# Kernel optimization log

Hardware: AMD Instinct MI355X
Metric: run time of the kernel (lower is better)

## Reference

```python
import jax, jax.numpy as jnp
import numpy as np

N_NODES = 50000
N_EDGES = 800000
F_IN, D1, N_CLS = 128, 128, 64


def gcn_conv(x, W, b, src, dst, n):
    # x: [N, Fin] -> linear transform then normalized scatter-add aggregation
    h = x @ W  # [N, Fout]
    deg = jnp.zeros((n,), h.dtype).at[dst].add(jnp.ones((dst.shape[0],), h.dtype))
    dis = jnp.where(deg > 0, jax.lax.rsqrt(jnp.maximum(deg, 1.0)), 0.0)  # deg^-1/2, inf->0
    norm = dis[src] * dis[dst]  # [E_tot]
    msgs = norm[:, None] * h[src]  # gather source features, scale by sym norm
    out = jax.ops.segment_sum(msgs, dst, num_segments=n)  # scatter-add to targets
    return out + b


def setup_inputs() -> dict:
    key = jax.random.key(0)
    ks = jax.random.split(key, 6)
    x = jax.random.normal(ks[0], (N_NODES, F_IN), dtype=jnp.float32)
    edge_index = jax.random.randint(ks[1], (2, N_EDGES), 0, N_NODES, dtype=jnp.int64)
    W1 = jax.random.normal(ks[2], (F_IN, D1), dtype=jnp.float32) / np.sqrt(F_IN)
    b1 = jnp.zeros((D1,), dtype=jnp.float32)
    W2 = jax.random.normal(ks[3], (D1, N_CLS), dtype=jnp.float32) / np.sqrt(D1)
    b2 = jnp.zeros((N_CLS,), dtype=jnp.float32)
    return {"x": x, "edge_index": edge_index, "W1": W1, "b1": b1, "W2": W2, "b2": b2}


def reference(x, edge_index, W1, b1, W2, b2):
    n = x.shape[0]
    loops = jnp.arange(n, dtype=edge_index.dtype)
    src = jnp.concatenate([edge_index[0], loops])  # add self-loops (PyG default)
    dst = jnp.concatenate([edge_index[1], loops])
    h = gcn_conv(x, W1, b1, src, dst, n)
    h = jax.nn.relu(h)
    # F.dropout(training=self.training) is identity in eval mode
    out = gcn_conv(h, W2, b2, src, dst, n)
    return out
```

## Files before the change

### kernel.cpp

```cpp
#include <hip/hip_runtime.h>

#define NN 50000
#define NE 800000
#define CAP 64
#define NPAD 50176
#define SLICE 6250

typedef unsigned int   u32;
typedef unsigned short u16;
typedef __attribute__((ext_vector_type(8))) short short8;
typedef __attribute__((ext_vector_type(4))) float f32x4;

__device__ inline u16 f2bf(float f) {
    u32 u = __float_as_uint(f);
    return (u16)((u + 0x7FFF + ((u >> 16) & 1)) >> 16);
}
__device__ inline float bfval(u16 h) { return __uint_as_float(((u32)h) << 16); }
__device__ inline float bf_lo(u32 u) { return __uint_as_float(u << 16); }
__device__ inline float bf_hi(u32 u) { return __uint_as_float(u & 0xFFFF0000u); }


__global__ __launch_bounds__(256) void build_ell(const int* __restrict__ ei,
                                                 int* __restrict__ cnt,
                                                 u16* __restrict__ ell) {
    const int s  = blockIdx.x & 7;
    const int g  = blockIdx.x >> 3;
    const int ng = gridDim.x >> 3;
    const int lo = s * SLICE, hi = lo + SLICE;
    for (int e0 = (g * 256 + (int)threadIdx.x) * 4; e0 < NE; e0 += ng * 1024) {
        int4 d4 = *(const int4*)(ei + NE + e0);
        int dv[4] = {d4.x, d4.y, d4.z, d4.w};
#pragma unroll
        for (int k = 0; k < 4; ++k) {
            int d = dv[k];
            if (d >= lo && d < hi) {
                int src = ei[e0 + k];
                int sh = k & 1;
                int pos = atomicAdd(&cnt[sh * NPAD + d], 1);
                if (pos < 32) ell[d * CAP + sh * 32 + pos] = (u16)src;
            }
        }
    }
}


__global__ __launch_bounds__(256) void prep_w(const float* __restrict__ W1,
                                              const float* __restrict__ W2,
                                              u16* __restrict__ W1h, u16* __restrict__ W1l,
                                              u16* __restrict__ W2h, u16* __restrict__ W2l,
                                              int* __restrict__ cnt) {
    int i = blockIdx.x * 256 + threadIdx.x;
    for (int z = i; z < 2 * NPAD; z += 32768) cnt[z] = 0;
    const float* W; u16 *Dh, *Dl; int NOUT, idx;
    if (i < 16384) { W = W1; Dh = W1h; Dl = W1l; NOUT = 128; idx = i; }
    else           { idx = i - 16384; if (idx >= 8192) return;
                     W = W2; Dh = W2h; Dl = W2l; NOUT = 64; }
    int j = idx & 7, l = (idx >> 3) & 63, kc = (idx >> 9) & 3, t = idx >> 11;
    int k = kc * 32 + (l >> 4) * 8 + j;
    int n = t * 16 + (l & 15);
    float w = W[k * NOUT + n];
    u16 h = f2bf(w);
    Dh[idx] = h;
    Dl[idx] = f2bf(w - bfval(h));
}


template <int NOUT>
__global__ __launch_bounds__(256) void gemm_mfma(const float* __restrict__ A,
                                                 const u16* __restrict__ Wh,
                                                 const u16* __restrict__ Wl,
                                                 u16* __restrict__ C, int M) {
    constexpr int NT = NOUT / 16;
    const int tid = threadIdx.x;
    const int w = tid >> 6, l = tid & 63;
    const int m = l & 15, q = l >> 4;

    int arow = blockIdx.x * 64 + w * 16 + m;
    const float* Ar = A + (size_t)min(arow, M - 1) * 128;

    f32x4 acc[NT] = {};

#pragma unroll
    for (int kc = 0; kc < 4; ++kc) {
        float p[8];
        *(float4*)&p[0] = *(const float4*)(Ar + kc * 32 + q * 8);
        *(float4*)&p[4] = *(const float4*)(Ar + kc * 32 + q * 8 + 4);
        short8 ah, al;
#pragma unroll
        for (int j = 0; j < 8; ++j) {
            u16 h = f2bf(p[j]);
            ah[j] = (short)h;
            al[j] = (short)f2bf(p[j] - bfval(h));
        }
#pragma unroll
        for (int t = 0; t < NT; ++t) {
            size_t bo = ((size_t)(t * 4 + kc) * 64 + l) * 8;
            short8 bh = *(const short8*)(Wh + bo);
            short8 bl = *(const short8*)(Wl + bo);
            acc[t] = __builtin_amdgcn_mfma_f32_16x16x32_bf16(ah, bh, acc[t], 0, 0, 0);
            acc[t] = __builtin_amdgcn_mfma_f32_16x16x32_bf16(al, bh, acc[t], 0, 0, 0);
            acc[t] = __builtin_amdgcn_mfma_f32_16x16x32_bf16(ah, bl, acc[t], 0, 0, 0);
        }
    }

    int growbase = blockIdx.x * 64 + w * 16 + q * 4;
#pragma unroll
    for (int t = 0; t < NT; ++t)
#pragma unroll
        for (int r = 0; r < 4; ++r) {
            int grow = growbase + r;
            if (grow < M) C[(size_t)grow * NOUT + t * 16 + m] = f2bf(acc[t][r]);
        }
}


__global__ __launch_bounds__(256) void gemm_mfma_bf(const u16* __restrict__ A,
                                                    const u16* __restrict__ Wh,
                                                    const u16* __restrict__ Wl,
                                                    u16* __restrict__ C, int M) {
    constexpr int NT = 4;
    const int tid = threadIdx.x;
    const int w = tid >> 6, l = tid & 63;
    const int m = l & 15, q = l >> 4;

    int arow = blockIdx.x * 64 + w * 16 + m;
    const u16* Ar = A + (size_t)min(arow, M - 1) * 128;

    f32x4 acc[NT] = {};

#pragma unroll
    for (int kc = 0; kc < 4; ++kc) {
        short8 ah = *(const short8*)(Ar + kc * 32 + q * 8);
#pragma unroll
        for (int t = 0; t < NT; ++t) {
            size_t bo = ((size_t)(t * 4 + kc) * 64 + l) * 8;
            short8 bh = *(const short8*)(Wh + bo);
            short8 bl = *(const short8*)(Wl + bo);
            acc[t] = __builtin_amdgcn_mfma_f32_16x16x32_bf16(ah, bh, acc[t], 0, 0, 0);
            acc[t] = __builtin_amdgcn_mfma_f32_16x16x32_bf16(ah, bl, acc[t], 0, 0, 0);
        }
    }

    int growbase = blockIdx.x * 64 + w * 16 + q * 4;
#pragma unroll
    for (int t = 0; t < NT; ++t)
#pragma unroll
        for (int r = 0; r < 4; ++r) {
            int grow = growbase + r;
            if (grow < M) C[(size_t)grow * 64 + t * 16 + m] = f2bf(acc[t][r]);
        }
}


template <int F, bool RELU, bool OUTBF>
__global__ __launch_bounds__(256) void aggregate(const u16* __restrict__ H,
                                                 const u16* __restrict__ ell,
                                                 const int* __restrict__ cnt,
                                                 const float* __restrict__ bias,
                                                 void* __restrict__ outp) {
    const int tid = threadIdx.x;
    const int node = (int)((blockIdx.x * 256 + tid) >> 6);
    if (node >= NN) return;
    const int lane = tid & 63;

    const int c0r = cnt[node], c1r = cnt[NPAD + node];
    const int c0 = min(c0r, 32), c1 = min(c1r, 32);
    const int ne = min(c0 + c1, 63);
    const float di = rsqrtf((float)(c0r + c1r + 1));
    int slot = (lane < c0) ? lane : 32 + (lane - c0);
    int   s_l = (lane < ne) ? (int)ell[(size_t)node * CAP + slot] : node;
    float n_l = (lane <= ne)
                    ? rsqrtf((float)(cnt[s_l] + cnt[NPAD + s_l] + 1)) * di
                    : 0.0f;

    constexpr int G = (F == 128) ? 4 : 8;
    constexpr int L = 64 / G;
    const int g = lane / L;
    const int ci = lane & (L - 1);

    const int m = ne + 1;
    const int mPad = (m + 2 * G - 1) & ~(2 * G - 1);

    float acc[8] = {0, 0, 0, 0, 0, 0, 0, 0};
    for (int j = 0; j < mPad; j += 2 * G) {
        int   sA = __shfl(s_l, j + g);
        float nA = __shfl(n_l, j + g);
        int   sB = __shfl(s_l, j + G + g);
        float nB = __shfl(n_l, j + G + g);
        uint4 vA = *(const uint4*)(H + (size_t)sA * F + ci * 8);
        uint4 vB = *(const uint4*)(H + (size_t)sB * F + ci * 8);
        acc[0] += nA * bf_lo(vA.x); acc[1] += nA * bf_hi(vA.x);
        acc[2] += nA * bf_lo(vA.y); acc[3] += nA * bf_hi(vA.y);
        acc[4] += nA * bf_lo(vA.z); acc[5] += nA * bf_hi(vA.z);
        acc[6] += nA * bf_lo(vA.w); acc[7] += nA * bf_hi(vA.w);
        acc[0] += nB * bf_lo(vB.x); acc[1] += nB * bf_hi(vB.x);
        acc[2] += nB * bf_lo(vB.y); acc[3] += nB * bf_hi(vB.y);
        acc[4] += nB * bf_lo(vB.z); acc[5] += nB * bf_hi(vB.z);
        acc[6] += nB * bf_lo(vB.w); acc[7] += nB * bf_hi(vB.w);
    }

#pragma unroll
    for (int i = 0; i < 8; ++i) {
        if (F == 64) acc[i] += __shfl_xor(acc[i], 8);
        acc[i] += __shfl_xor(acc[i], 16);
        acc[i] += __shfl_xor(acc[i], 32);
    }

    const int active = (F == 128) ? 32 : 16;
    if (lane < active) {
        int part, c0i;
        if (F == 128) { part = lane >> 4;       c0i = (lane & 15) * 8 + part * 4; }
        else          { part = (lane >> 3) & 1; c0i = (lane & 7) * 8 + part * 4; }
        float4 b4 = *(const float4*)(bias + c0i);
        float4 o = make_float4(acc[part * 4 + 0] + b4.x, acc[part * 4 + 1] + b4.y,
                               acc[part * 4 + 2] + b4.z, acc[part * 4 + 3] + b4.w);
        if (RELU) { o.x = fmaxf(o.x, 0.f); o.y = fmaxf(o.y, 0.f);
                    o.z = fmaxf(o.z, 0.f); o.w = fmaxf(o.w, 0.f); }
        if (OUTBF) {
            u16* out = (u16*)outp;
            *(ushort4*)(out + (size_t)node * F + c0i) =
                make_ushort4(f2bf(o.x), f2bf(o.y), f2bf(o.z), f2bf(o.w));
        } else {
            float* out = (float*)outp;
            *(float4*)(out + (size_t)node * F + c0i) = o;
        }
    }
}


extern "C" void kernel_launch(void* const* d_in, const int* in_sizes, int n_in,
                              void* d_out, int out_size, void* d_ws, size_t ws_size,
                              hipStream_t stream) {
    const float* x  = (const float*)d_in[0];
    const int*   ei = (const int*)d_in[1];
    const float* W1 = (const float*)d_in[2];
    const float* b1 = (const float*)d_in[3];
    const float* W2 = (const float*)d_in[4];
    const float* b2 = (const float*)d_in[5];
    float* out = (float*)d_out;

    char* ws = (char*)d_ws;
    size_t off = 0;
    int* cnt = (int*)ws;                     off += (size_t)2 * NPAD * 4;
    u16* ell = (u16*)(ws + off);             off += (size_t)NN * CAP * 2;
    off = (off + 255) & ~(size_t)255;
    u16* W1h = (u16*)(ws + off);             off += 16384 * 2;
    u16* W1l = (u16*)(ws + off);             off += 16384 * 2;
    u16* W2h = (u16*)(ws + off);             off += 8192 * 2;
    u16* W2l = (u16*)(ws + off);             off += 8192 * 2;
    off = (off + 255) & ~(size_t)255;
    u16* Hbf = (u16*)(ws + off);             off += (size_t)NN * 128 * 2;
    u16* Abf = (u16*)(ws + off);             off += (size_t)NN * 128 * 2;

    prep_w<<<128, 256, 0, stream>>>(W1, W2, W1h, W1l, W2h, W2l, cnt);
    build_ell<<<1600, 256, 0, stream>>>(ei, cnt, ell);

    gemm_mfma<128><<<(NN + 63) / 64, 256, 0, stream>>>(x, W1h, W1l, Hbf, NN);
    aggregate<128, true, true><<<(NN + 3) / 4, 256, 0, stream>>>(Hbf, ell, cnt, b1, Abf);

    gemm_mfma_bf<<<(NN + 63) / 64, 256, 0, stream>>>(Abf, W2h, W2l, Hbf, NN);
    aggregate<64, false, false><<<(NN + 3) / 4, 256, 0, stream>>>(Hbf, ell, cnt, b2, out);
}
```

Measured before the change: 196.9 us.

## Fuse all GCN stages into one cooperative persistent kernel with grid syncs

Replaces the six separate launches with a single cooperative kernel that uses grid-wide syncs between stages. Half the blocks build the ELL adjacency while the other half run the first GEMM at the same time, and the later stages loop over tiles in persistent-block fashion. The aim is to remove launch gaps and overlap the atomic-heavy graph build with MFMA work. The cost is four grid barriers and a grid capped at 512 blocks, which may reduce occupancy and latency hiding in the gather-heavy aggregation.

Measured after the change: 520.7 us. 164% more time.

```diff
diff --git a/kernel.cpp b/kernel.cpp
--- a/kernel.cpp
+++ b/kernel.cpp
@@ -1,10 +1,14 @@
 #include <hip/hip_runtime.h>
+#include <hip/hip_cooperative_groups.h>
+
+namespace cg = cooperative_groups;
 
 #define NN 50000
 #define NE 800000
 #define CAP 64
 #define NPAD 50176
 #define SLICE 6250
+#define NTILE 782
 
 typedef unsigned int   u32;
 typedef unsigned short u16;
@@ -20,66 +24,44 @@
 __device__ inline float bf_hi(u32 u) { return __uint_as_float(u & 0xFFFF0000u); }
 
 
-__global__ __launch_bounds__(256) void build_ell(const int* __restrict__ ei,
-                                                 int* __restrict__ cnt,
-                                                 u16* __restrict__ ell) {
-    const int s  = blockIdx.x & 7;
-    const int g  = blockIdx.x >> 3;
-    const int ng = gridDim.x >> 3;
+__device__ inline void dev_build(int b, int BB, int tid,
+                                 const int* __restrict__ ei,
+                                 int* __restrict__ cnt,
+                                 u16* __restrict__ ell) {
+    const int s  = b & 7;
+    const int g  = b >> 3;
+    const int ng = BB >> 3;
     const int lo = s * SLICE, hi = lo + SLICE;
-    for (int e0 = (g * 256 + (int)threadIdx.x) * 4; e0 < NE; e0 += ng * 1024) {
+    for (int e0 = (g * 256 + tid) * 4; e0 < NE; e0 += ng * 1024) {
         int4 d4 = *(const int4*)(ei + NE + e0);
+        int4 s4 = *(const int4*)(ei + e0);
         int dv[4] = {d4.x, d4.y, d4.z, d4.w};
+        int sv[4] = {s4.x, s4.y, s4.z, s4.w};
 #pragma unroll
         for (int k = 0; k < 4; ++k) {
             int d = dv[k];
             if (d >= lo && d < hi) {
-                int src = ei[e0 + k];
                 int sh = k & 1;
                 int pos = atomicAdd(&cnt[sh * NPAD + d], 1);
-                if (pos < 32) ell[d * CAP + sh * 32 + pos] = (u16)src;
+                if (pos < 32) ell[d * CAP + sh * 32 + pos] = (u16)sv[k];
             }
         }
     }
 }
 
 
-__global__ __launch_bounds__(256) void prep_w(const float* __restrict__ W1,
-                                              const float* __restrict__ W2,
-                                              u16* __restrict__ W1h, u16* __restrict__ W1l,
-                                              u16* __restrict__ W2h, u16* __restrict__ W2l,
-                                              int* __restrict__ cnt) {
-    int i = blockIdx.x * 256 + threadIdx.x;
-    for (int z = i; z < 2 * NPAD; z += 32768) cnt[z] = 0;
-    const float* W; u16 *Dh, *Dl; int NOUT, idx;
-    if (i < 16384) { W = W1; Dh = W1h; Dl = W1l; NOUT = 128; idx = i; }
-    else           { idx = i - 16384; if (idx >= 8192) return;
-                     W = W2; Dh = W2h; Dl = W2l; NOUT = 64; }
-    int j = idx & 7, l = (idx >> 3) & 63, kc = (idx >> 9) & 3, t = idx >> 11;
-    int k = kc * 32 + (l >> 4) * 8 + j;
-    int n = t * 16 + (l & 15);
-    float w = W[k * NOUT + n];
-    u16 h = f2bf(w);
-    Dh[idx] = h;
-    Dl[idx] = f2bf(w - bfval(h));
-}
-
-
-template <int NOUT>
-__global__ __launch_bounds__(256) void gemm_mfma(const float* __restrict__ A,
-                                                 const u16* __restrict__ Wh,
-                                                 const u16* __restrict__ Wl,
-                                                 u16* __restrict__ C, int M) {
-    constexpr int NT = NOUT / 16;
-    const int tid = threadIdx.x;
+__device__ inline void dev_gemm1_tile(int t, int tid,
+                                      const float* __restrict__ A,
+                                      const u16* __restrict__ Wh,
+                                      const u16* __restrict__ Wl,
+                                      u16* __restrict__ C) {
     const int w = tid >> 6, l = tid & 63;
     const int m = l & 15, q = l >> 4;
 
-    int arow = blockIdx.x * 64 + w * 16 + m;
-    const float* Ar = A + (size_t)min(arow, M - 1) * 128;
-
-    f32x4 acc[NT] = {};
-
+    int arow = t * 64 + w * 16 + m;
+    const float* Ar = A + (size_t)min(arow, NN - 1) * 128;
+
+    f32x4 acc[8] = {};
 #pragma unroll
     for (int kc = 0; kc < 4; ++kc) {
         float p[8];
@@ -93,75 +75,69 @@
             al[j] = (short)f2bf(p[j] - bfval(h));
         }
 #pragma unroll
-        for (int t = 0; t < NT; ++t) {
-            size_t bo = ((size_t)(t * 4 + kc) * 64 + l) * 8;
+        for (int t2 = 0; t2 < 8; ++t2) {
+            size_t bo = ((size_t)(t2 * 4 + kc) * 64 + l) * 8;
             short8 bh = *(const short8*)(Wh + bo);
             short8 bl = *(const short8*)(Wl + bo);
-            acc[t] = __builtin_amdgcn_mfma_f32_16x16x32_bf16(ah, bh, acc[t], 0, 0, 0);
-            acc[t] = __builtin_amdgcn_mfma_f32_16x16x32_bf16(al, bh, acc[t], 0, 0, 0);
-            acc[t] = __builtin_amdgcn_mfma_f32_16x16x32_bf16(ah, bl, acc[t], 0, 0, 0);
-        }
-    }
-
-    int growbase = blockIdx.x * 64 + w * 16 + q * 4;
-#pragma unroll
-    for (int t = 0; t < NT; ++t)
+            acc[t2] = __builtin_amdgcn_mfma_f32_16x16x32_bf16(ah, bh, acc[t2], 0, 0, 0);
+            acc[t2] = __builtin_amdgcn_mfma_f32_16x16x32_bf16(al, bh, acc[t2], 0, 0, 0);
+            acc[t2] = __builtin_amdgcn_mfma_f32_16x16x32_bf16(ah, bl, acc[t2], 0, 0, 0);
+        }
+    }
+    int growbase = t * 64 + w * 16 + q * 4;
+#pragma unroll
+    for (int t2 = 0; t2 < 8; ++t2)
 #pragma unroll
         for (int r = 0; r < 4; ++r) {
             int grow = growbase + r;
-            if (grow < M) C[(size_t)grow * NOUT + t * 16 + m] = f2bf(acc[t][r]);
-        }
-}
-
-
-__global__ __launch_bounds__(256) void gemm_mfma_bf(const u16* __restrict__ A,
-                                                    const u16* __restrict__ Wh,
-                                                    const u16* __restrict__ Wl,
-                                                    u16* __restrict__ C, int M) {
-    constexpr int NT = 4;
-    const int tid = threadIdx.x;
+            if (grow < NN) C[(size_t)grow * 128 + t2 * 16 + m] = f2bf(acc[t2][r]);
+        }
+}
+
+
+__device__ inline void dev_gemm2_tile(int t, int tid,
+                                      const u16* __restrict__ A,
+                                      const u16* __restrict__ Wh,
+                                      const u16* __restrict__ Wl,
+                                      u16* __restrict__ C) {
     const int w = tid >> 6, l = tid & 63;
     const int m = l & 15, q = l >> 4;
 
-    int arow = blockIdx.x * 64 + w * 16 + m;
-    const u16* Ar = A + (size_t)min(arow, M - 1) * 128;
-
-    f32x4 acc[NT] = {};
-
+    int arow = t * 64 + w * 16 + m;
+    const u16* Ar = A + (size_t)min(arow, NN - 1) * 128;
+
+    f32x4 acc[4] = {};
 #pragma unroll
     for (int kc = 0; kc < 4; ++kc) {
         short8 ah = *(const short8*)(Ar + kc * 32 + q * 8);
 #pragma unroll
-        for (int t = 0; t < NT; ++t) {
-            size_t bo = ((size_t)(t * 4 + kc) * 64 + l) * 8;
+        for (int t2 = 0; t2 < 4; ++t2) {
+            size_t bo = ((size_t)(t2 * 4 + kc) * 64 + l) * 8;
             short8 bh = *(const short8*)(Wh + bo);
             short8 bl = *(const short8*)(Wl + bo);
-            acc[t] = __builtin_amdgcn_mfma_f32_16x16x32_bf16(ah, bh, acc[t], 0, 0, 0);
-            acc[t] = __builtin_amdgcn_mfma_f32_16x16x32_bf16(ah, bl, acc[t], 0, 0, 0);
-        }
-    }
-
-    int growbase = blockIdx.x * 64 + w * 16 + q * 4;
-#pragma unroll
-    for (int t = 0; t < NT; ++t)
+            acc[t2] = __builtin_amdgcn_mfma_f32_16x16x32_bf16(ah, bh, acc[t2], 0, 0, 0);
+            acc[t2] = __builtin_amdgcn_mfma_f32_16x16x32_bf16(ah, bl, acc[t2], 0, 0, 0);
+        }
+    }
+    int growbase = t * 64 + w * 16 + q * 4;
+#pragma unroll
+    for (int t2 = 0; t2 < 4; ++t2)
 #pragma unroll
         for (int r = 0; r < 4; ++r) {
             int grow = growbase + r;
-            if (grow < M) C[(size_t)grow * 64 + t * 16 + m] = f2bf(acc[t][r]);
+            if (grow < NN) C[(size_t)grow * 64 + t2 * 16 + m] = f2bf(acc[t2][r]);
         }
 }
 
 
 template <int F, bool RELU, bool OUTBF>
-__global__ __launch_bounds__(256) void aggregate(const u16* __restrict__ H,
-                                                 const u16* __restrict__ ell,
-                                                 const int* __restrict__ cnt,
-                                                 const float* __restrict__ bias,
-                                                 void* __restrict__ outp) {
-    const int tid = threadIdx.x;
-    const int node = (int)((blockIdx.x * 256 + tid) >> 6);
+__device__ inline void dev_agg(int node, int lane,
+                               const u16* __restrict__ H,
+                               const u16* __restrict__ ell,
+                               const int* __restrict__ cnt,
+                               const float* __restrict__ bias,
+                               void* __restrict__ outp) {
     if (node >= NN) return;
-    const int lane = tid & 63;
 
     const int c0r = cnt[node], c1r = cnt[NPAD + node];
     const int c0 = min(c0r, 32), c1 = min(c1r, 32);
@@ -228,6 +204,59 @@
 }
 
 
+__global__ __launch_bounds__(256, 2) void fused(
+        const float* __restrict__ x, const int* __restrict__ ei,
+        const float* __restrict__ W1, const float* __restrict__ b1,
+        const float* __restrict__ W2, const float* __restrict__ b2,
+        float* __restrict__ out,
+        int* __restrict__ cnt, u16* __restrict__ ell,
+        u16* __restrict__ W1h, u16* __restrict__ W1l,
+        u16* __restrict__ W2h, u16* __restrict__ W2l,
+        u16* __restrict__ Hbf, u16* __restrict__ Abf) {
+    cg::grid_group grid = cg::this_grid();
+    const int b = blockIdx.x, tid = threadIdx.x;
+    const int NB = gridDim.x;
+    const int nthreads = NB * 256;
+    const int gi = b * 256 + tid;
+    const int lane = tid & 63;
+
+    for (int z = gi; z < 2 * NPAD; z += nthreads) cnt[z] = 0;
+    for (int idx0 = gi; idx0 < 24576; idx0 += nthreads) {
+        const float* W; u16 *Dh, *Dl; int NOUT, idx;
+        if (idx0 < 16384) { W = W1; Dh = W1h; Dl = W1l; NOUT = 128; idx = idx0; }
+        else              { W = W2; Dh = W2h; Dl = W2l; NOUT = 64;  idx = idx0 - 16384; }
+        int j = idx & 7, l = (idx >> 3) & 63, kc = (idx >> 9) & 3, t = idx >> 11;
+        int k = kc * 32 + (l >> 4) * 8 + j;
+        int n = t * 16 + (l & 15);
+        float w = W[k * NOUT + n];
+        u16 h = f2bf(w);
+        Dh[idx] = h;
+        Dl[idx] = f2bf(w - bfval(h));
+    }
+    grid.sync();
+
+    const int BB = NB >> 1;
+    if (b < BB) {
+        dev_build(b, BB, tid, ei, cnt, ell);
+    } else {
+        for (int t = b - BB; t < NTILE; t += NB - BB)
+            dev_gemm1_tile(t, tid, x, W1h, W1l, Hbf);
+    }
+    grid.sync();
+
+    for (int gb = b; gb < (NN + 3) / 4; gb += NB)
+        dev_agg<128, true, true>(gb * 4 + (tid >> 6), lane, Hbf, ell, cnt, b1, Abf);
+    grid.sync();
+
+    for (int t = b; t < NTILE; t += NB)
+        dev_gemm2_tile(t, tid, Abf, W2h, W2l, Hbf);
+    grid.sync();
+
+    for (int gb = b; gb < (NN + 3) / 4; gb += NB)
+        dev_agg<64, false, false>(gb * 4 + (tid >> 6), lane, Hbf, ell, cnt, b2, out);
+}
+
+
 extern "C" void kernel_launch(void* const* d_in, const int* in_sizes, int n_in,
                               void* d_out, int out_size, void* d_ws, size_t ws_size,
                               hipStream_t stream) {
@@ -252,12 +281,16 @@
     u16* Hbf = (u16*)(ws + off);             off += (size_t)NN * 128 * 2;
     u16* Abf = (u16*)(ws + off);             off += (size_t)NN * 128 * 2;
 
-    prep_w<<<128, 256, 0, stream>>>(W1, W2, W1h, W1l, W2h, W2l, cnt);
-    build_ell<<<1600, 256, 0, stream>>>(ei, cnt, ell);
-
-    gemm_mfma<128><<<(NN + 63) / 64, 256, 0, stream>>>(x, W1h, W1l, Hbf, NN);
-    aggregate<128, true, true><<<(NN + 3) / 4, 256, 0, stream>>>(Hbf, ell, cnt, b1, Abf);
-
-    gemm_mfma_bf<<<(NN + 63) / 64, 256, 0, stream>>>(Abf, W2h, W2l, Hbf, NN);
-    aggregate<64, false, false><<<(NN + 3) / 4, 256, 0, stream>>>(Hbf, ell, cnt, b2, out);
-}
+    int nb = 2;
+    hipOccupancyMaxActiveBlocksPerMultiprocessor(&nb, fused, 256, 0);
+    if (nb < 1) nb = 1;
+    int grid = nb * 256;
+    if (grid > 512) grid = 512;
+    grid &= ~15;
+    if (grid < 16) grid = 16;
+
+    void* params[] = {&x, &ei, &W1, &b1, &W2, &b2, &out,
+                      &cnt, &ell, &W1h, &W1l, &W2h, &W2l, &Hbf, &Abf};
+    hipLaunchCooperativeKernel((void*)fused, dim3(grid), dim3(256),
+                               params, 0, stream);
+}
```

## Split features into 32-column chunks and aggregate per chunk with packed edge lists

Applied to the files above, without the earlier changes.

Stores GEMM outputs in a chunked layout (32 features per chunk, one contiguous plane per chunk). Aggregation then runs one pass per chunk, so each gathered plane is smaller and more likely to stay in L2. A new pack_edges kernel precomputes each edge's source index and fp16 norm into one 32-bit word, which removes the per-aggregation recomputation of the norms. The cost is more launches, more edge-list reads (once per pass), 16-byte-per-lane gathers, fp16 precision on the norms, and an extra kernel plus workspace.

After: 269.6 us. 36.9% more time.

```diff
diff --git a/kernel.cpp b/kernel.cpp
--- a/kernel.cpp
+++ b/kernel.cpp
@@ -1,4 +1,5 @@
 #include <hip/hip_runtime.h>
+#include <hip/hip_fp16.h>
 
 #define NN 50000
 #define NE 800000
@@ -29,15 +30,16 @@
     const int lo = s * SLICE, hi = lo + SLICE;
     for (int e0 = (g * 256 + (int)threadIdx.x) * 4; e0 < NE; e0 += ng * 1024) {
         int4 d4 = *(const int4*)(ei + NE + e0);
+        int4 s4 = *(const int4*)(ei + e0);
         int dv[4] = {d4.x, d4.y, d4.z, d4.w};
+        int sv[4] = {s4.x, s4.y, s4.z, s4.w};
 #pragma unroll
         for (int k = 0; k < 4; ++k) {
             int d = dv[k];
             if (d >= lo && d < hi) {
-                int src = ei[e0 + k];
                 int sh = k & 1;
                 int pos = atomicAdd(&cnt[sh * NPAD + d], 1);
-                if (pos < 32) ell[d * CAP + sh * 32 + pos] = (u16)src;
+                if (pos < 32) ell[d * CAP + sh * 32 + pos] = (u16)sv[k];
             }
         }
     }
@@ -65,21 +67,41 @@
 }
 
 
-template <int NOUT>
-__global__ __launch_bounds__(256) void gemm_mfma(const float* __restrict__ A,
-                                                 const u16* __restrict__ Wh,
-                                                 const u16* __restrict__ Wl,
-                                                 u16* __restrict__ C, int M) {
-    constexpr int NT = NOUT / 16;
+__global__ __launch_bounds__(256) void pack_edges(const u16* __restrict__ ell,
+                                                  const int* __restrict__ cnt,
+                                                  u32* __restrict__ epk) {
+    const int tid = threadIdx.x;
+    const int node = blockIdx.x * 4 + (tid >> 6);
+    if (node >= NN) return;
+    const int lane = tid & 63;
+    const int c0r = cnt[node], c1r = cnt[NPAD + node];
+    const int c0 = min(c0r, 32), c1 = min(c1r, 32);
+    const int ne = min(c0 + c1, 63);
+    const float di = rsqrtf((float)(c0r + c1r + 1));
+    if (lane > ne) return;
+    int s; float nr;
+    if (lane < ne) {
+        int slot = (lane < c0) ? lane : 32 + (lane - c0);
+        s = (int)ell[(size_t)node * CAP + slot];
+        nr = rsqrtf((float)(cnt[s] + cnt[NPAD + s] + 1)) * di;
+    } else { s = node; nr = di * di; }
+    epk[(size_t)node * CAP + lane] =
+        (u32)s | ((u32)__half_as_ushort(__float2half_rn(nr)) << 16);
+}
+
+
+__global__ __launch_bounds__(256) void gemm1(const float* __restrict__ A,
+                                             const u16* __restrict__ Wh,
+                                             const u16* __restrict__ Wl,
+                                             u16* __restrict__ C) {
     const int tid = threadIdx.x;
     const int w = tid >> 6, l = tid & 63;
     const int m = l & 15, q = l >> 4;
 
     int arow = blockIdx.x * 64 + w * 16 + m;
-    const float* Ar = A + (size_t)min(arow, M - 1) * 128;
-
-    f32x4 acc[NT] = {};
-
+    const float* Ar = A + (size_t)min(arow, NN - 1) * 128;
+
+    f32x4 acc[8] = {};
 #pragma unroll
     for (int kc = 0; kc < 4; ++kc) {
         float p[8];
@@ -93,136 +115,127 @@
             al[j] = (short)f2bf(p[j] - bfval(h));
         }
 #pragma unroll
-        for (int t = 0; t < NT; ++t) {
-            size_t bo = ((size_t)(t * 4 + kc) * 64 + l) * 8;
+        for (int t2 = 0; t2 < 8; ++t2) {
+            size_t bo = ((size_t)(t2 * 4 + kc) * 64 + l) * 8;
             short8 bh = *(const short8*)(Wh + bo);
             short8 bl = *(const short8*)(Wl + bo);
-            acc[t] = __builtin_amdgcn_mfma_f32_16x16x32_bf16(ah, bh, acc[t], 0, 0, 0);
-            acc[t] = __builtin_amdgcn_mfma_f32_16x16x32_bf16(al, bh, acc[t], 0, 0, 0);
-            acc[t] = __builtin_amdgcn_mfma_f32_16x16x32_bf16(ah, bl, acc[t], 0, 0, 0);
-        }
-    }
-
+            acc[t2] = __builtin_amdgcn_mfma_f32_16x16x32_bf16(ah, bh, acc[t2], 0, 0, 0);
+            acc[t2] = __builtin_amdgcn_mfma_f32_16x16x32_bf16(al, bh, acc[t2], 0, 0, 0);
+            acc[t2] = __builtin_amdgcn_mfma_f32_16x16x32_bf16(ah, bl, acc[t2], 0, 0, 0);
+        }
+    }
     int growbase = blockIdx.x * 64 + w * 16 + q * 4;
 #pragma unroll
-    for (int t = 0; t < NT; ++t)
+    for (int t2 = 0; t2 < 8; ++t2)
 #pragma unroll
         for (int r = 0; r < 4; ++r) {
             int grow = growbase + r;
-            if (grow < M) C[(size_t)grow * NOUT + t * 16 + m] = f2bf(acc[t][r]);
-        }
-}
-
-
-__global__ __launch_bounds__(256) void gemm_mfma_bf(const u16* __restrict__ A,
-                                                    const u16* __restrict__ Wh,
-                                                    const u16* __restrict__ Wl,
-                                                    u16* __restrict__ C, int M) {
-    constexpr int NT = 4;
+            if (grow < NN)
+                C[((size_t)(t2 >> 1) * NN + grow) * 32 + (t2 & 1) * 16 + m] =
+                    f2bf(acc[t2][r]);
+        }
+}
+
+
+__global__ __launch_bounds__(256) void gemm2(const u16* __restrict__ A,
+                                             const u16* __restrict__ Wh,
+                                             const u16* __restrict__ Wl,
+                                             u16* __restrict__ C) {
     const int tid = threadIdx.x;
     const int w = tid >> 6, l = tid & 63;
     const int m = l & 15, q = l >> 4;
 
-    int arow = blockIdx.x * 64 + w * 16 + m;
-    const u16* Ar = A + (size_t)min(arow, M - 1) * 128;
-
-    f32x4 acc[NT] = {};
-
+    int arow = min(blockIdx.x * 64 + w * 16 + m, NN - 1);
+
+    f32x4 acc[4] = {};
 #pragma unroll
     for (int kc = 0; kc < 4; ++kc) {
-        short8 ah = *(const short8*)(Ar + kc * 32 + q * 8);
-#pragma unroll
-        for (int t = 0; t < NT; ++t) {
-            size_t bo = ((size_t)(t * 4 + kc) * 64 + l) * 8;
+        short8 ah = *(const short8*)(A + ((size_t)kc * NN + arow) * 32 + q * 8);
+#pragma unroll
+        for (int t2 = 0; t2 < 4; ++t2) {
+            size_t bo = ((size_t)(t2 * 4 + kc) * 64 + l) * 8;
             short8 bh = *(const short8*)(Wh + bo);
             short8 bl = *(const short8*)(Wl + bo);
-            acc[t] = __builtin_amdgcn_mfma_f32_16x16x32_bf16(ah, bh, acc[t], 0, 0, 0);
-            acc[t] = __builtin_amdgcn_mfma_f32_16x16x32_bf16(ah, bl, acc[t], 0, 0, 0);
-        }
-    }
-
+            acc[t2] = __builtin_amdgcn_mfma_f32_16x16x32_bf16(ah, bh, acc[t2], 0, 0, 0);
+            acc[t2] = __builtin_amdgcn_mfma_f32_16x16x32_bf16(ah, bl, acc[t2], 0, 0, 0);
+        }
+    }
     int growbase = blockIdx.x * 64 + w * 16 + q * 4;
 #pragma unroll
-    for (int t = 0; t < NT; ++t)
+    for (int t2 = 0; t2 < 4; ++t2)
 #pragma unroll
         for (int r = 0; r < 4; ++r) {
             int grow = growbase + r;
-            if (grow < M) C[(size_t)grow * 64 + t * 16 + m] = f2bf(acc[t][r]);
-        }
-}
-
-
-template <int F, bool RELU, bool OUTBF>
-__global__ __launch_bounds__(256) void aggregate(const u16* __restrict__ H,
-                                                 const u16* __restrict__ ell,
-                                                 const int* __restrict__ cnt,
-                                                 const float* __restrict__ bias,
-                                                 void* __restrict__ outp) {
-    const int tid = threadIdx.x;
-    const int node = (int)((blockIdx.x * 256 + tid) >> 6);
+            if (grow < NN)
+                C[((size_t)(t2 >> 1) * NN + grow) * 32 + (t2 & 1) * 16 + m] =
+                    f2bf(acc[t2][r]);
+        }
+}
+
+
+template <int NPASS, bool RELU, bool OUTBF>
+__global__ __launch_bounds__(256) void agg_pass(const u32* __restrict__ epk,
+                                                const int* __restrict__ cnt,
+                                                const u16* __restrict__ T,
+                                                const float* __restrict__ bias,
+                                                void* __restrict__ outp) {
+    const int tid = threadIdx.x;
+    const int p = blockIdx.x / 12500;
+    const int node = (blockIdx.x % 12500) * 4 + (tid >> 6);
     if (node >= NN) return;
     const int lane = tid & 63;
 
     const int c0r = cnt[node], c1r = cnt[NPAD + node];
-    const int c0 = min(c0r, 32), c1 = min(c1r, 32);
-    const int ne = min(c0 + c1, 63);
-    const float di = rsqrtf((float)(c0r + c1r + 1));
-    int slot = (lane < c0) ? lane : 32 + (lane - c0);
-    int   s_l = (lane < ne) ? (int)ell[(size_t)node * CAP + slot] : node;
-    float n_l = (lane <= ne)
-                    ? rsqrtf((float)(cnt[s_l] + cnt[NPAD + s_l] + 1)) * di
+    const int ne = min(min(c0r, 32) + min(c1r, 32), 63);
+    const int m = ne + 1;
+
+    u32 e = (lane < m) ? epk[(size_t)node * CAP + lane] : (u32)node;
+    int   s_l = (int)(e & 0xFFFF);
+    float n_l = (lane < m)
+                    ? __half2float(__ushort_as_half((u16)(e >> 16)))
                     : 0.0f;
 
-    constexpr int G = (F == 128) ? 4 : 8;
-    constexpr int L = 64 / G;
-    const int g = lane / L;
-    const int ci = lane & (L - 1);
-
-    const int m = ne + 1;
-    const int mPad = (m + 2 * G - 1) & ~(2 * G - 1);
+    const u16* Tp = T + (size_t)p * NN * 32;
+    const int g  = lane >> 2;
+    const int ci = lane & 3;
 
     float acc[8] = {0, 0, 0, 0, 0, 0, 0, 0};
-    for (int j = 0; j < mPad; j += 2 * G) {
-        int   sA = __shfl(s_l, j + g);
-        float nA = __shfl(n_l, j + g);
-        int   sB = __shfl(s_l, j + G + g);
-        float nB = __shfl(n_l, j + G + g);
-        uint4 vA = *(const uint4*)(H + (size_t)sA * F + ci * 8);
-        uint4 vB = *(const uint4*)(H + (size_t)sB * F + ci * 8);
-        acc[0] += nA * bf_lo(vA.x); acc[1] += nA * bf_hi(vA.x);
-        acc[2] += nA * bf_lo(vA.y); acc[3] += nA * bf_hi(vA.y);
-        acc[4] += nA * bf_lo(vA.z); acc[5] += nA * bf_hi(vA.z);
-        acc[6] += nA * bf_lo(vA.w); acc[7] += nA * bf_hi(vA.w);
-        acc[0] += nB * bf_lo(vB.x); acc[1] += nB * bf_hi(vB.x);
-        acc[2] += nB * bf_lo(vB.y); acc[3] += nB * bf_hi(vB.y);
-        acc[4] += nB * bf_lo(vB.z); acc[5] += nB * bf_hi(vB.z);
-        acc[6] += nB * bf_lo(vB.w); acc[7] += nB * bf_hi(vB.w);
+    const int mPad = (m + 15) & ~15;
+    for (int j = 0; j < mPad; j += 16) {
+        int   sE = __shfl(s_l, j + g);
+        float nE = __shfl(n_l, j + g);
+        uint4 v = *(const uint4*)(Tp + (size_t)sE * 32 + ci * 8);
+        acc[0] += nE * bf_lo(v.x); acc[1] += nE * bf_hi(v.x);
+        acc[2] += nE * bf_lo(v.y); acc[3] += nE * bf_hi(v.y);
+        acc[4] += nE * bf_lo(v.z); acc[5] += nE * bf_hi(v.z);
+        acc[6] += nE * bf_lo(v.w); acc[7] += nE * bf_hi(v.w);
     }
 
 #pragma unroll
     for (int i = 0; i < 8; ++i) {
-        if (F == 64) acc[i] += __shfl_xor(acc[i], 8);
+        acc[i] += __shfl_xor(acc[i], 4);
+        acc[i] += __shfl_xor(acc[i], 8);
         acc[i] += __shfl_xor(acc[i], 16);
         acc[i] += __shfl_xor(acc[i], 32);
     }
 
-    const int active = (F == 128) ? 32 : 16;
-    if (lane < active) {
-        int part, c0i;
-        if (F == 128) { part = lane >> 4;       c0i = (lane & 15) * 8 + part * 4; }
-        else          { part = (lane >> 3) & 1; c0i = (lane & 7) * 8 + part * 4; }
-        float4 b4 = *(const float4*)(bias + c0i);
-        float4 o = make_float4(acc[part * 4 + 0] + b4.x, acc[part * 4 + 1] + b4.y,
-                               acc[part * 4 + 2] + b4.z, acc[part * 4 + 3] + b4.w);
-        if (RELU) { o.x = fmaxf(o.x, 0.f); o.y = fmaxf(o.y, 0.f);
-                    o.z = fmaxf(o.z, 0.f); o.w = fmaxf(o.w, 0.f); }
+    if (lane < 4) {
+        float4 b0 = *(const float4*)(bias + p * 32 + ci * 8);
+        float4 b1 = *(const float4*)(bias + p * 32 + ci * 8 + 4);
+        float o[8] = {acc[0] + b0.x, acc[1] + b0.y, acc[2] + b0.z, acc[3] + b0.w,
+                      acc[4] + b1.x, acc[5] + b1.y, acc[6] + b1.z, acc[7] + b1.w};
+        if (RELU)
+#pragma unroll
+            for (int i = 0; i < 8; ++i) o[i] = fmaxf(o[i], 0.f);
         if (OUTBF) {
-            u16* out = (u16*)outp;
-            *(ushort4*)(out + (size_t)node * F + c0i) =
-                make_ushort4(f2bf(o.x), f2bf(o.y), f2bf(o.z), f2bf(o.w));
+            short8 ov;
+#pragma unroll
+            for (int i = 0; i < 8; ++i) ov[i] = (short)f2bf(o[i]);
+            *(short8*)((u16*)outp + ((size_t)p * NN + node) * 32 + ci * 8) = ov;
         } else {
-            float* out = (float*)outp;
-            *(float4*)(out + (size_t)node * F + c0i) = o;
+            float* out = (float*)outp + (size_t)node * (NPASS * 32) + p * 32 + ci * 8;
+            *(float4*)out       = make_float4(o[0], o[1], o[2], o[3]);
+            *(float4*)(out + 4) = make_float4(o[4], o[5], o[6], o[7]);
         }
     }
 }
@@ -244,20 +257,23 @@
     int* cnt = (int*)ws;                     off += (size_t)2 * NPAD * 4;
     u16* ell = (u16*)(ws + off);             off += (size_t)NN * CAP * 2;
     off = (off + 255) & ~(size_t)255;
+    u32* epk = (u32*)(ws + off);             off += (size_t)NN * CAP * 4;
     u16* W1h = (u16*)(ws + off);             off += 16384 * 2;
     u16* W1l = (u16*)(ws + off);             off += 16384 * 2;
     u16* W2h = (u16*)(ws + off);             off += 8192 * 2;
     u16* W2l = (u16*)(ws + off);             off += 8192 * 2;
     off = (off + 255) & ~(size_t)255;
-    u16* Hbf = (u16*)(ws + off);             off += (size_t)NN * 128 * 2;
-    u16* Abf = (u16*)(ws + off);             off += (size_t)NN * 128 * 2;
+    u16* H1c = (u16*)(ws + off);             off += (size_t)4 * NN * 32 * 2;
+    u16* A1c = (u16*)(ws + off);             off += (size_t)4 * NN * 32 * 2;
+    u16* H2c = (u16*)(ws + off);             off += (size_t)2 * NN * 32 * 2;
 
     prep_w<<<128, 256, 0, stream>>>(W1, W2, W1h, W1l, W2h, W2l, cnt);
     build_ell<<<1600, 256, 0, stream>>>(ei, cnt, ell);
-
-    gemm_mfma<128><<<(NN + 63) / 64, 256, 0, stream>>>(x, W1h, W1l, Hbf, NN);
-    aggregate<128, true, true><<<(NN + 3) / 4, 256, 0, stream>>>(Hbf, ell, cnt, b1, Abf);
-
-    gemm_mfma_bf<<<(NN + 63) / 64, 256, 0, stream>>>(Abf, W2h, W2l, Hbf, NN);
-    aggregate<64, false, false><<<(NN + 3) / 4, 256, 0, stream>>>(Hbf, ell, cnt, b2, out);
-}
+    pack_edges<<<12500, 256, 0, stream>>>(ell, cnt, epk);
+
+    gemm1<<<(NN + 63) / 64, 256, 0, stream>>>(x, W1h, W1l, H1c);
+    agg_pass<4, true, true><<<4 * 12500, 256, 0, stream>>>(epk, cnt, H1c, b1, A1c);
+
+    gemm2<<<(NN + 63) / 64, 256, 0, stream>>>(A1c, W2h, W2l, H2c);
+    agg_pass<2, false, false><<<2 * 12500, 256, 0, stream>>>(epk, cnt, H2c, b2, out);
+}
```

## Precompute packed edge index and fp16 norm once, batch ELL build atomics

Applied to the files above, without the earlier changes.

Adds a pack_edges pass that computes each node's neighbor list with its symmetric normalization coefficient, packed as a 16-bit index plus an fp16 weight in one u32, along with a per-node edge count. Both aggregate passes now read this packed array instead of recomputing counts and doing dependent cnt gathers for every neighbor. build_ell loads sixteen edges per thread up front and issues its atomics back to back so their latency overlaps. The extra kernel and the larger edge buffer add memory traffic, and storing the norm in fp16 slightly reduces its precision.

New measurement: 210.9 us. 7.1% more time.

```diff
diff --git a/kernel.cpp b/kernel.cpp
--- a/kernel.cpp
+++ b/kernel.cpp
@@ -1,4 +1,5 @@
 #include <hip/hip_runtime.h>
+#include <hip/hip_fp16.h>
 
 #define NN 50000
 #define NE 800000
@@ -23,24 +24,35 @@
 __global__ __launch_bounds__(256) void build_ell(const int* __restrict__ ei,
                                                  int* __restrict__ cnt,
                                                  u16* __restrict__ ell) {
-    const int s  = blockIdx.x & 7;
-    const int g  = blockIdx.x >> 3;
-    const int ng = gridDim.x >> 3;
+    const int s = blockIdx.x & 7;
+    const int g = blockIdx.x >> 3;
+    const int u = g * 256 + (int)threadIdx.x;
     const int lo = s * SLICE, hi = lo + SLICE;
-    for (int e0 = (g * 256 + (int)threadIdx.x) * 4; e0 < NE; e0 += ng * 1024) {
-        int4 d4 = *(const int4*)(ei + NE + e0);
-        int dv[4] = {d4.x, d4.y, d4.z, d4.w};
-#pragma unroll
-        for (int k = 0; k < 4; ++k) {
-            int d = dv[k];
-            if (d >= lo && d < hi) {
-                int src = ei[e0 + k];
-                int sh = k & 1;
-                int pos = atomicAdd(&cnt[sh * NPAD + d], 1);
-                if (pos < 32) ell[d * CAP + sh * 32 + pos] = (u16)src;
-            }
-        }
-    }
+
+    int dv[16], sv[16];
+#pragma unroll
+    for (int k = 0; k < 4; ++k) {
+        int e0 = (u + k * 51200) * 4;
+        if (e0 < NE) {
+            *(int4*)&dv[k * 4] = *(const int4*)(ei + NE + e0);
+            *(int4*)&sv[k * 4] = *(const int4*)(ei + e0);
+        } else {
+#pragma unroll
+            for (int j = 0; j < 4; ++j) { dv[k * 4 + j] = -1; sv[k * 4 + j] = 0; }
+        }
+    }
+
+    int pos[16];
+#pragma unroll
+    for (int k = 0; k < 16; ++k) {
+        pos[k] = -1;
+        if (dv[k] >= lo && dv[k] < hi)
+            pos[k] = atomicAdd(&cnt[(k & 1) * NPAD + dv[k]], 1);
+    }
+#pragma unroll
+    for (int k = 0; k < 16; ++k)
+        if (pos[k] >= 0 && pos[k] < 32)
+            ell[dv[k] * CAP + (k & 1) * 32 + pos[k]] = (u16)sv[k];
 }
 
 
@@ -65,21 +77,43 @@
 }
 
 
-template <int NOUT>
-__global__ __launch_bounds__(256) void gemm_mfma(const float* __restrict__ A,
-                                                 const u16* __restrict__ Wh,
-                                                 const u16* __restrict__ Wl,
-                                                 u16* __restrict__ C, int M) {
-    constexpr int NT = NOUT / 16;
+__global__ __launch_bounds__(256) void pack_edges(const u16* __restrict__ ell,
+                                                  const int* __restrict__ cnt,
+                                                  u32* __restrict__ epk,
+                                                  u16* __restrict__ degm) {
+    const int tid = threadIdx.x;
+    const int node = blockIdx.x * 4 + (tid >> 6);
+    if (node >= NN) return;
+    const int lane = tid & 63;
+    const int c0r = cnt[node], c1r = cnt[NPAD + node];
+    const int c0 = min(c0r, 32), c1 = min(c1r, 32);
+    const int ne = min(c0 + c1, 63);
+    const float di = rsqrtf((float)(c0r + c1r + 1));
+    if (lane == 0) degm[node] = (u16)(ne + 1);
+    if (lane > ne) return;
+    int s; float nr;
+    if (lane < ne) {
+        int slot = (lane < c0) ? lane : 32 + (lane - c0);
+        s = (int)ell[(size_t)node * CAP + slot];
+        nr = rsqrtf((float)(cnt[s] + cnt[NPAD + s] + 1)) * di;
+    } else { s = node; nr = di * di; }
+    epk[(size_t)node * CAP + lane] =
+        (u32)s | ((u32)__half_as_ushort(__float2half_rn(nr)) << 16);
+}
+
+
+__global__ __launch_bounds__(256) void gemm1(const float* __restrict__ A,
+                                             const u16* __restrict__ Wh,
+                                             const u16* __restrict__ Wl,
+                                             u16* __restrict__ C) {
     const int tid = threadIdx.x;
     const int w = tid >> 6, l = tid & 63;
     const int m = l & 15, q = l >> 4;
 
     int arow = blockIdx.x * 64 + w * 16 + m;
-    const float* Ar = A + (size_t)min(arow, M - 1) * 128;
-
-    f32x4 acc[NT] = {};
-
+    const float* Ar = A + (size_t)min(arow, NN - 1) * 128;
+
+    f32x4 acc[8] = {};
 #pragma unroll
     for (int kc = 0; kc < 4; ++kc) {
         float p[8];
@@ -93,69 +127,65 @@
             al[j] = (short)f2bf(p[j] - bfval(h));
         }
 #pragma unroll
-        for (int t = 0; t < NT; ++t) {
-            size_t bo = ((size_t)(t * 4 + kc) * 64 + l) * 8;
+        for (int t2 = 0; t2 < 8; ++t2) {
+            size_t bo = ((size_t)(t2 * 4 + kc) * 64 + l) * 8;
             short8 bh = *(const short8*)(Wh + bo);
             short8 bl = *(const short8*)(Wl + bo);
-            acc[t] = __builtin_amdgcn_mfma_f32_16x16x32_bf16(ah, bh, acc[t], 0, 0, 0);
-            acc[t] = __builtin_amdgcn_mfma_f32_16x16x32_bf16(al, bh, acc[t], 0, 0, 0);
-            acc[t] = __builtin_amdgcn_mfma_f32_16x16x32_bf16(ah, bl, acc[t], 0, 0, 0);
-        }
-    }
-
+            acc[t2] = __builtin_amdgcn_mfma_f32_16x16x32_bf16(ah, bh, acc[t2], 0, 0, 0);
+            acc[t2] = __builtin_amdgcn_mfma_f32_16x16x32_bf16(al, bh, acc[t2], 0, 0, 0);
+            acc[t2] = __builtin_amdgcn_mfma_f32_16x16x32_bf16(ah, bl, acc[t2], 0, 0, 0);
+        }
+    }
     int growbase = blockIdx.x * 64 + w * 16 + q * 4;
 #pragma unroll
-    for (int t = 0; t < NT; ++t)
+    for (int t2 = 0; t2 < 8; ++t2)
 #pragma unroll
         for (int r = 0; r < 4; ++r) {
             int grow = growbase + r;
-            if (grow < M) C[(size_t)grow * NOUT + t * 16 + m] = f2bf(acc[t][r]);
-        }
-}
-
-
-__global__ __launch_bounds__(256) void gemm_mfma_bf(const u16* __restrict__ A,
-                                                    const u16* __restrict__ Wh,
-                                                    const u16* __restrict__ Wl,
-                                                    u16* __restrict__ C, int M) {
-    constexpr int NT = 4;
+            if (grow < NN) C[(size_t)grow * 128 + t2 * 16 + m] = f2bf(acc[t2][r]);
+        }
+}
+
+
+__global__ __launch_bounds__(256) void gemm2(const u16* __restrict__ A,
+                                             const u16* __restrict__ Wh,
+                                             const u16* __restrict__ Wl,
+                                             u16* __restrict__ C) {
     const int tid = threadIdx.x;
     const int w = tid >> 6, l = tid & 63;
     const int m = l & 15, q = l >> 4;
 
-    int arow = blockIdx.x * 64 + w * 16 + m;
-    const u16* Ar = A + (size_t)min(arow, M - 1) * 128;
-
-    f32x4 acc[NT] = {};
-
+    int arow = min(blockIdx.x * 64 + w * 16 + m, NN - 1);
+    const u16* Ar = A + (size_t)arow * 128;
+
+    f32x4 acc[4] = {};
 #pragma unroll
     for (int kc = 0; kc < 4; ++kc) {
         short8 ah = *(const short8*)(Ar + kc * 32 + q * 8);
 #pragma unroll
-        for (int t = 0; t < NT; ++t) {
-            size_t bo = ((size_t)(t * 4 + kc) * 64 + l) * 8;
+        for (int t2 = 0; t2 < 4; ++t2) {
+            size_t bo = ((size_t)(t2 * 4 + kc) * 64 + l) * 8;
             short8 bh = *(const short8*)(Wh + bo);
             short8 bl = *(const short8*)(Wl + bo);
-            acc[t] = __builtin_amdgcn_mfma_f32_16x16x32_bf16(ah, bh, acc[t], 0, 0, 0);
-            acc[t] = __builtin_amdgcn_mfma_f32_16x16x32_bf16(ah, bl, acc[t], 0, 0, 0);
-        }
-    }
-
+            acc[t2] = __builtin_amdgcn_mfma_f32_16x16x32_bf16(ah, bh, acc[t2], 0, 0, 0);
+            acc[t2] = __builtin_amdgcn_mfma_f32_16x16x32_bf16(ah, bl, acc[t2], 0, 0, 0);
+        }
+    }
     int growbase = blockIdx.x * 64 + w * 16 + q * 4;
 #pragma unroll
-    for (int t = 0; t < NT; ++t)
+    for (int t2 = 0; t2 < 4; ++t2)
 #pragma unroll
         for (int r = 0; r < 4; ++r) {
             int grow = growbase + r;
-            if (grow < M) C[(size_t)grow * 64 + t * 16 + m] = f2bf(acc[t][r]);
+            if (grow < NN) C[(size_t)grow * 64 + t2 * 16 + m] = f2bf(acc[t2][r]);
         }
 }
 
 
 template <int F, bool RELU, bool OUTBF>
 __global__ __launch_bounds__(256) void aggregate(const u16* __restrict__ H,
-                                                 const u16* __restrict__ ell,
-                                                 const int* __restrict__ cnt,
+                                                 const u32* __restrict__ epk,
+                                                 const u16* __restrict__ degm,
                                                  const float* __restrict__ bias,
                                                  void* __restrict__ outp) {
     const int tid = threadIdx.x;
@@ -163,14 +193,11 @@
     if (node >= NN) return;
     const int lane = tid & 63;
 
-    const int c0r = cnt[node], c1r = cnt[NPAD + node];
-    const int c0 = min(c0r, 32), c1 = min(c1r, 32);
-    const int ne = min(c0 + c1, 63);
-    const float di = rsqrtf((float)(c0r + c1r + 1));
-    int slot = (lane < c0) ? lane : 32 + (lane - c0);
-    int   s_l = (lane < ne) ? (int)ell[(size_t)node * CAP + slot] : node;
-    float n_l = (lane <= ne)
-                    ? rsqrtf((float)(cnt[s_l] + cnt[NPAD + s_l] + 1)) * di
+    const int m = (int)degm[node];
+    u32 e = (lane < m) ? epk[(size_t)node * CAP + lane] : (u32)node;
+    int   s_l = (int)(e & 0xFFFF);
+    float n_l = (lane < m)
+                    ? __half2float(__ushort_as_half((u16)(e >> 16)))
                     : 0.0f;
 
     constexpr int G = (F == 128) ? 4 : 8;
@@ -178,7 +205,6 @@
     const int g = lane / L;
     const int ci = lane & (L - 1);
 
-    const int m = ne + 1;
     const int mPad = (m + 2 * G - 1) & ~(2 * G - 1);
 
     float acc[8] = {0, 0, 0, 0, 0, 0, 0, 0};
@@ -244,6 +270,9 @@
     int* cnt = (int*)ws;                     off += (size_t)2 * NPAD * 4;
     u16* ell = (u16*)(ws + off);             off += (size_t)NN * CAP * 2;
     off = (off + 255) & ~(size_t)255;
+    u32* epk = (u32*)(ws + off);             off += (size_t)NN * CAP * 4;
+    u16* degm = (u16*)(ws + off);            off += (size_t)NN * 2;
+    off = (off + 255) & ~(size_t)255;
     u16* W1h = (u16*)(ws + off);             off += 16384 * 2;
     u16* W1l = (u16*)(ws + off);             off += 16384 * 2;
     u16* W2h = (u16*)(ws + off);             off += 8192 * 2;
@@ -254,10 +283,11 @@
 
     prep_w<<<128, 256, 0, stream>>>(W1, W2, W1h, W1l, W2h, W2l, cnt);
     build_ell<<<1600, 256, 0, stream>>>(ei, cnt, ell);
-
-    gemm_mfma<128><<<(NN + 63) / 64, 256, 0, stream>>>(x, W1h, W1l, Hbf, NN);
-    aggregate<128, true, true><<<(NN + 3) / 4, 256, 0, stream>>>(Hbf, ell, cnt, b1, Abf);
-
-    gemm_mfma_bf<<<(NN + 63) / 64, 256, 0, stream>>>(Abf, W2h, W2l, Hbf, NN);
-    aggregate<64, false, false><<<(NN + 3) / 4, 256, 0, stream>>>(Hbf, ell, cnt, b2, out);
-}
+    pack_edges<<<12500, 256, 0, stream>>>(ell, cnt, epk, degm);
+
+    gemm1<<<(NN + 63) / 64, 256, 0, stream>>>(x, W1h, W1l, Hbf);
+    aggregate<128, true, true><<<(NN + 3) / 4, 256, 0, stream>>>(Hbf, epk, degm, b1, Abf);
+
+    gemm2<<<(NN + 63) / 64, 256, 0, stream>>>(Abf, W2h, W2l, Hbf);
+    aggregate<64, false, false><<<(NN + 3) / 4, 256, 0, stream>>>(Hbf, epk, degm, b2, out);
+}
```
